# Performance work log

Measured on AMD Instinct MI355X. Metric: run time of the kernel, lower is better.

## Reference

```python
import jax, jax.numpy as jnp
import numpy as np
import math

NUM_HEADS = 16
HEAD_DIM = 64
D_MODEL = NUM_HEADS * HEAD_DIM  # 1024
B, S = 4, 2048

def setup_inputs() -> dict:
    key = jax.random.key(0)
    ks = jax.random.split(key, 8)
    sd = 1.0 / math.sqrt(D_MODEL)
    return {
        "hidden_states": jax.random.normal(ks[0], (B, S, D_MODEL), jnp.float32),
        "attention_mask": jnp.zeros((B, 1, 1, S), jnp.float32),
        "Wq": jax.random.normal(ks[1], (D_MODEL, D_MODEL), jnp.float32) * sd,
        "bq": jnp.zeros((D_MODEL,), jnp.float32),
        "Wk": jax.random.normal(ks[2], (D_MODEL, D_MODEL), jnp.float32) * sd,
        "bk": jnp.zeros((D_MODEL,), jnp.float32),
        "Wv": jax.random.normal(ks[3], (D_MODEL, D_MODEL), jnp.float32) * sd,
        "bv": jnp.zeros((D_MODEL,), jnp.float32),
    }

def _split_heads(x):
    # [B, S, D] -> [B, H, S, hd]
    b, s, _ = x.shape
    return x.reshape(b, s, NUM_HEADS, HEAD_DIM).transpose(0, 2, 1, 3)

def reference(hidden_states, attention_mask, Wq, bq, Wk, bk, Wv, bv):
    # Linear projections (torch nn.Linear: x @ W.T + b)
    q = _split_heads(hidden_states @ Wq.T + bq)
    k = _split_heads(hidden_states @ Wk.T + bk)
    v = _split_heads(hidden_states @ Wv.T + bv)
    scale = 1.0 / math.sqrt(HEAD_DIM)
    # [B, H, Sq, Sk] attention scores, fully materialized as in the original
    scores = jnp.einsum("bhqd,bhkd->bhqk", q, k) * scale + attention_mask
    # relusq replacement for softmax
    probs = jnp.square(jax.nn.relu(scores))
    ctx = jnp.einsum("bhqk,bhkd->bhqd", probs, v)  # [B, H, S, hd]
    b = ctx.shape[0]
    return ctx.transpose(0, 2, 1, 3).reshape(b, -1, D_MODEL)
```

## Files before the change

### kernel.cpp

```cpp
#include <hip/hip_runtime.h>


typedef __bf16 bf16x8 __attribute__((ext_vector_type(8)));
typedef __bf16 bf16x4 __attribute__((ext_vector_type(4)));
typedef short  s16x4  __attribute__((ext_vector_type(4)));
typedef float  f32x4  __attribute__((ext_vector_type(4)));
typedef float  floatx4 __attribute__((ext_vector_type(4)));

#define MFMA16(a, b, c) __builtin_amdgcn_mfma_f32_16x16x32_bf16(a, b, c, 0, 0, 0)
#define MFMA16K16(a, b, c) \
    __builtin_amdgcn_mfma_f32_16x16x16bf16_1k(a, b, c, 0, 0, 0)

#define WAITCNT_VM0() __builtin_amdgcn_s_waitcnt(0x0F70)
#define WAITCNT_VM2() __builtin_amdgcn_s_waitcnt(0x0F72)
#define BARRIER() __builtin_amdgcn_s_barrier()
#define SETPRIO(p) __builtin_amdgcn_s_setprio(p)

__device__ __forceinline__ void glds16(const __bf16* g, __bf16* l) {
    __builtin_amdgcn_global_load_lds(
        (const __attribute__((address_space(1))) void*)g,
        (__attribute__((address_space(3))) void*)l, 16, 0, 0);
}

__global__ __launch_bounds__(256) void convert_kernel(
    const float* __restrict__ X, const float* __restrict__ Wq,
    const float* __restrict__ Wk, const float* __restrict__ Wv,
    __bf16* __restrict__ Xb, __bf16* __restrict__ Wqb,
    __bf16* __restrict__ Wkb, __bf16* __restrict__ Wvb)
{
    int blk = blockIdx.x;
    const float* src; __bf16* dst; size_t base;
    if (blk < 4096)      { src = X;  dst = Xb;  base = (size_t)blk * 2048; }
    else if (blk < 4608) { src = Wq; dst = Wqb; base = (size_t)(blk - 4096) * 2048; }
    else if (blk < 5120) { src = Wk; dst = Wkb; base = (size_t)(blk - 4608) * 2048; }
    else                 { src = Wv; dst = Wvb; base = (size_t)(blk - 5120) * 2048; }
    size_t off = base + (size_t)threadIdx.x * 8;
    floatx4 a = *(const floatx4*)(src + off);
    floatx4 c = *(const floatx4*)(src + off + 4);
    bf16x8 o;
    o[0] = (__bf16)a[0]; o[1] = (__bf16)a[1]; o[2] = (__bf16)a[2]; o[3] = (__bf16)a[3];
    o[4] = (__bf16)c[0]; o[5] = (__bf16)c[1]; o[6] = (__bf16)c[2]; o[7] = (__bf16)c[3];
    *(bf16x8*)(dst + off) = o;
}

__global__ __launch_bounds__(256) void qkv_gemm_kernel(
    const __bf16* __restrict__ Xb,
    const __bf16* __restrict__ Wqb, const __bf16* __restrict__ Wkb,
    const __bf16* __restrict__ Wvb,
    const float* __restrict__ bq, const float* __restrict__ bk,
    const float* __restrict__ bv,
    __bf16* __restrict__ qws, __bf16* __restrict__ kws, __bf16* __restrict__ vws)
{
    __shared__ __bf16 As[2][128 * 64];
    __shared__ __bf16 Bs[2][128 * 64];

    const int tid  = threadIdx.x;
    const int lane = tid & 63;
    const int wave = tid >> 6;
    const int wm   = (wave >> 1) * 64;
    const int wn   = (wave & 1) * 64;
    const int quad = lane >> 4;
    const int l16  = lane & 15;
    const int m0   = blockIdx.y * 128;

    const int sel = blockIdx.x >> 3;
    const bool vmode = (sel == 2);
    const __bf16* Wb = (sel == 0) ? Wqb : (sel == 1) ? Wkb : Wvb;
    const float* bias = (sel == 0) ? bq : (sel == 1) ? bk : bv;
    __bf16* outp = (sel == 0) ? qws : (sel == 1) ? kws : vws;
    const int n0 = (blockIdx.x & 7) * 128;

    const int woffA = vmode ? wm : wn;
    const int woffB = vmode ? wn : wm;

    const int srow = lane >> 3;
    const int schk = lane & 7;

    f32x4 acc[4][4] = {};

    #pragma unroll
    for (int i = 0; i < 4; ++i) {
        int rb = wave * 32 + i * 8;
        int r  = rb + srow;
        int c  = schk ^ (r & 7);
        glds16(Xb + (size_t)(m0 + r) * 1024 + c * 8, &As[0][rb * 64]);
        glds16(Wb + (size_t)(n0 + r) * 1024 + c * 8, &Bs[0][rb * 64]);
    }
    WAITCNT_VM0();
    BARRIER();

    for (int s = 0; s < 16; ++s) {
        const int kn = ((s + 1) & 15) * 64;
        const int nb = (s + 1) & 1;
        const int bc = s & 1;
        #pragma unroll
        for (int i = 0; i < 4; ++i) {
            int rb = wave * 32 + i * 8;
            int r  = rb + srow;
            int c  = schk ^ (r & 7);
            glds16(Xb + (size_t)(m0 + r) * 1024 + kn + c * 8, &As[nb][rb * 64]);
            glds16(Wb + (size_t)(n0 + r) * 1024 + kn + c * 8, &Bs[nb][rb * 64]);
        }

        const __bf16* Pa_ = vmode ? &As[bc][0] : &Bs[bc][0];
        const __bf16* Pb_ = vmode ? &Bs[bc][0] : &As[bc][0];

        SETPRIO(1);
        #pragma unroll
        for (int kk8 = 0; kk8 < 8; kk8 += 4) {
            bf16x8 af[4], bfr[4];
            #pragma unroll
            for (int a = 0; a < 4; ++a)
                af[a] = *(const bf16x8*)&Pa_[(woffA + a * 16 + l16) * 64 +
                                             (((kk8 + quad) ^ (l16 & 7)) * 8)];
            #pragma unroll
            for (int bb = 0; bb < 4; ++bb)
                bfr[bb] = *(const bf16x8*)&Pb_[(woffB + bb * 16 + l16) * 64 +
                                               (((kk8 + quad) ^ (l16 & 7)) * 8)];
            #pragma unroll
            for (int a = 0; a < 4; ++a)
                #pragma unroll
                for (int bb = 0; bb < 4; ++bb)
                    acc[a][bb] = MFMA16(af[a], bfr[bb], acc[a][bb]);
        }
        SETPRIO(0);

        WAITCNT_VM0();
        BARRIER();
    }

    if (!vmode) {
        #pragma unroll
        for (int a = 0; a < 4; ++a) {
            int n = n0 + woffA + a * 16 + quad * 4;
            floatx4 bv4 = *(const floatx4*)&bias[n];
            int h = n >> 6, d0 = n & 63;
            #pragma unroll
            for (int bb = 0; bb < 4; ++bb) {
                int m = m0 + woffB + bb * 16 + l16;
                int bt = m >> 11, ss = m & 2047;
                bf16x4 o;
                #pragma unroll
                for (int r = 0; r < 4; ++r)
                    o[r] = (__bf16)(acc[a][bb][r] + bv4[r]);
                *(bf16x4*)&outp[((size_t)(bt * 16 + h) * 2048 + ss) * 64 + d0] = o;
            }
        }
    } else {
        #pragma unroll
        for (int a = 0; a < 4; ++a) {
            int m = m0 + woffA + a * 16 + quad * 4;
            int bt = m >> 11, s0 = m & 2047;
            #pragma unroll
            for (int bb = 0; bb < 4; ++bb) {
                int n = n0 + woffB + bb * 16 + l16;
                float bvv = bias[n];
                int h = n >> 6, d = n & 63;
                bf16x4 o;
                #pragma unroll
                for (int r = 0; r < 4; ++r)
                    o[r] = (__bf16)(acc[a][bb][r] + bvv);
                *(bf16x4*)&outp[((size_t)(bt * 16 + h) * 64 + d) * 2048 + s0] = o;
            }
        }
    }
}

__global__ __launch_bounds__(512, 4) void attn_kernel(
    const __bf16* __restrict__ Q, const __bf16* __restrict__ K,
    const __bf16* __restrict__ Vt, const float* __restrict__ mask,
    float* __restrict__ out)
{
    __shared__ __bf16 Ks[2][64 * 64];
    __shared__ __bf16 Vs[2][64 * 64];
    __shared__ float  Ms[2048];

    const int tid  = threadIdx.x;
    const int lane = tid & 63;
    const int wave = tid >> 6;
    const int quad = lane >> 4;
    const int l16  = lane & 15;
    const int bh   = blockIdx.x;
    const int b    = bh >> 4;
    const int h    = bh & 15;
    const int q0   = blockIdx.y * 256 + wave * 32;

    const __bf16* Qb = Q  + (size_t)bh * 2048 * 64;
    const __bf16* Kb = K  + (size_t)bh * 2048 * 64;
    const __bf16* Vb = Vt + (size_t)bh * 64 * 2048;
    const float*  mb = mask + b * 2048;

    const int rb = wave * 8;
    const int sr = rb + (lane >> 3);
    const int sc = ((lane & 7) ^ (sr & 7)) * 8;

    bf16x8 aq[2][2];
    #pragma unroll
    for (int qi = 0; qi < 2; ++qi)
        #pragma unroll
        for (int kcd = 0; kcd < 2; ++kcd)
            aq[qi][kcd] = *(const bf16x8*)(Qb +
                (size_t)(q0 + qi * 16 + l16) * 64 + kcd * 32 + quad * 8);

    f32x4 co[2][4] = {};

    glds16(Kb + (size_t)sr * 64 + sc, &Ks[0][rb * 64]);
    glds16(Vb + (size_t)sr * 2048 + sc, &Vs[0][rb * 64]);
    glds16((const __bf16*)mb + (size_t)wave * 512 + lane * 8,
           (__bf16*)Ms + wave * 512);

    for (int t = 0; t < 32; ++t) {
        const int k0 = t * 64;
        const int kn = ((t + 1) & 31) * 64;
        const int nb = (t + 1) & 1;
        glds16(Kb + (size_t)(kn + sr) * 64 + sc, &Ks[nb][rb * 64]);
        glds16(Vb + (size_t)sr * 2048 + kn + sc, &Vs[nb][rb * 64]);
        WAITCNT_VM2();
        BARRIER();

        const __bf16* Kt = &Ks[t & 1][0];
        const __bf16* Vtile = &Vs[t & 1][0];

        f32x4 st[4][2] = {};
        SETPRIO(1);
        #pragma unroll
        for (int ki = 0; ki < 4; ++ki) {
            #pragma unroll
            for (int kcd = 0; kcd < 2; ++kcd) {
                int key = ki * 16 + l16;
                bf16x8 ak = *(const bf16x8*)&Kt[key * 64 +
                    (((kcd * 4 + quad) ^ (key & 7)) * 8)];
                #pragma unroll
                for (int qi = 0; qi < 2; ++qi)
                    st[ki][qi] = MFMA16(ak, aq[qi][kcd], st[ki][qi]);
            }
        }
        SETPRIO(0);

        bf16x4 pf[4][2];
        const f32x4 zero4 = {};
        #pragma unroll
        for (int ki = 0; ki < 4; ++ki) {
            f32x4 mk = *(const f32x4*)&Ms[k0 + ki * 16 + quad * 4];
            #pragma unroll
            for (int qi = 0; qi < 2; ++qi) {
                f32x4 x = st[ki][qi] * 0.125f + mk;
                x = __builtin_elementwise_max(x, zero4);
                x = x * x;
                bf16x4 pv;
                pv[0] = (__bf16)x[0]; pv[1] = (__bf16)x[1];
                pv[2] = (__bf16)x[2]; pv[3] = (__bf16)x[3];
                pf[ki][qi] = pv;
            }
        }

        SETPRIO(1);
        #pragma unroll
        for (int ki = 0; ki < 4; ++ki) {
            bf16x4 vb4[4];
            #pragma unroll
            for (int dt = 0; dt < 4; ++dt) {
                int d = dt * 16 + l16;
                int g = ki * 2 + (quad >> 1);
                vb4[dt] = *(const bf16x4*)&Vtile[d * 64 +
                    ((g ^ (d & 7)) * 8) + (quad & 1) * 4];
            }
            #pragma unroll
            for (int qi = 0; qi < 2; ++qi) {
                s16x4 pa = __builtin_bit_cast(s16x4, pf[ki][qi]);
                #pragma unroll
                for (int dt = 0; dt < 4; ++dt)
                    co[qi][dt] = MFMA16K16(pa,
                        __builtin_bit_cast(s16x4, vb4[dt]), co[qi][dt]);
            }
        }
        SETPRIO(0);
        BARRIER();
    }

    #pragma unroll
    for (int qi = 0; qi < 2; ++qi)
        #pragma unroll
        for (int r = 0; r < 4; ++r) {
            int q = q0 + qi * 16 + quad * 4 + r;
            float* orow = &out[(((size_t)b * 2048 + q) * 16 + h) * 64];
            #pragma unroll
            for (int dt = 0; dt < 4; ++dt)
                orow[dt * 16 + l16] = co[qi][dt][r];
        }
}

extern "C" void kernel_launch(void* const* d_in, const int* in_sizes, int n_in,
                              void* d_out, int out_size, void* d_ws, size_t ws_size,
                              hipStream_t stream) {
    const float* hidden = (const float*)d_in[0];
    const float* mask   = (const float*)d_in[1];
    const float* Wq     = (const float*)d_in[2];
    const float* bq     = (const float*)d_in[3];
    const float* Wk     = (const float*)d_in[4];
    const float* bk     = (const float*)d_in[5];
    const float* Wv     = (const float*)d_in[6];
    const float* bv     = (const float*)d_in[7];
    float* out = (float*)d_out;

    __bf16* qws = (__bf16*)d_ws;
    __bf16* kws = qws + (size_t)64 * 2048 * 64;
    __bf16* vws = kws + (size_t)64 * 2048 * 64;
    __bf16* Xb  = vws + (size_t)64 * 2048 * 64;
    __bf16* Wqb = Xb  + (size_t)8192 * 1024;
    __bf16* Wkb = Wqb + (size_t)1024 * 1024;
    __bf16* Wvb = Wkb + (size_t)1024 * 1024;

    convert_kernel<<<dim3(5632), dim3(256), 0, stream>>>(hidden, Wq, Wk, Wv,
                                                         Xb, Wqb, Wkb, Wvb);
    qkv_gemm_kernel<<<dim3(24, 64), dim3(256), 0, stream>>>(Xb, Wqb, Wkb, Wvb,
                                                            bq, bk, bv,
                                                            qws, kws, vws);
    attn_kernel<<<dim3(64, 8), dim3(512), 0, stream>>>(qws, kws, vws, mask, out);
}
```

Before: 250.2 us.

## Double-buffer 128-key K/V tiles with one barrier per iteration in attention

The attention loop now stages two 64-key K and V sub-tiles per iteration, so it runs 16 iterations instead of 32. Prefetch for the next 128 keys is issued at the top of the loop and waited on at the bottom, with one barrier per iteration, so the global loads can overlap a full iteration of MFMA work instead of being waited on right away. This halves the barrier and waitcnt count. In exchange LDS use doubles to 64KB for K/V plus 8KB for the mask, which may cut the number of resident blocks per CU below the launch-bounds target of 4.

```diff
diff --git a/kernel.cpp b/kernel.cpp
--- a/kernel.cpp
+++ b/kernel.cpp
@@ -12,7 +12,6 @@
     __builtin_amdgcn_mfma_f32_16x16x16bf16_1k(a, b, c, 0, 0, 0)
 
 #define WAITCNT_VM0() __builtin_amdgcn_s_waitcnt(0x0F70)
-#define WAITCNT_VM2() __builtin_amdgcn_s_waitcnt(0x0F72)
 #define BARRIER() __builtin_amdgcn_s_barrier()
 #define SETPRIO(p) __builtin_amdgcn_s_setprio(p)
 
@@ -171,8 +170,8 @@
     const __bf16* __restrict__ Vt, const float* __restrict__ mask,
     float* __restrict__ out)
 {
-    __shared__ __bf16 Ks[2][64 * 64];
-    __shared__ __bf16 Vs[2][64 * 64];
+    __shared__ __bf16 Ks[2][2][64 * 64];
+    __shared__ __bf16 Vs[2][2][64 * 64];
     __shared__ float  Ms[2048];
 
     const int tid  = threadIdx.x;
@@ -204,77 +203,87 @@
 
     f32x4 co[2][4] = {};
 
-    glds16(Kb + (size_t)sr * 64 + sc, &Ks[0][rb * 64]);
-    glds16(Vb + (size_t)sr * 2048 + sc, &Vs[0][rb * 64]);
+    glds16(Kb + (size_t)sr * 64 + sc,        &Ks[0][0][rb * 64]);
+    glds16(Kb + (size_t)(64 + sr) * 64 + sc, &Ks[0][1][rb * 64]);
+    glds16(Vb + (size_t)sr * 2048 + sc,      &Vs[0][0][rb * 64]);
+    glds16(Vb + (size_t)sr * 2048 + 64 + sc, &Vs[0][1][rb * 64]);
     glds16((const __bf16*)mb + (size_t)wave * 512 + lane * 8,
            (__bf16*)Ms + wave * 512);
-
-    for (int t = 0; t < 32; ++t) {
-        const int k0 = t * 64;
-        const int kn = ((t + 1) & 31) * 64;
+    WAITCNT_VM0();
+    BARRIER();
+
+    for (int t = 0; t < 16; ++t) {
+        const int kn = ((t + 1) & 15) * 128;
         const int nb = (t + 1) & 1;
-        glds16(Kb + (size_t)(kn + sr) * 64 + sc, &Ks[nb][rb * 64]);
-        glds16(Vb + (size_t)sr * 2048 + kn + sc, &Vs[nb][rb * 64]);
-        WAITCNT_VM2();
-        BARRIER();
-
-        const __bf16* Kt = &Ks[t & 1][0];
-        const __bf16* Vtile = &Vs[t & 1][0];
-
-        f32x4 st[4][2] = {};
-        SETPRIO(1);
-        #pragma unroll
-        for (int ki = 0; ki < 4; ++ki) {
-            #pragma unroll
-            for (int kcd = 0; kcd < 2; ++kcd) {
-                int key = ki * 16 + l16;
-                bf16x8 ak = *(const bf16x8*)&Kt[key * 64 +
-                    (((kcd * 4 + quad) ^ (key & 7)) * 8)];
-                #pragma unroll
-                for (int qi = 0; qi < 2; ++qi)
-                    st[ki][qi] = MFMA16(ak, aq[qi][kcd], st[ki][qi]);
-            }
-        }
-        SETPRIO(0);
-
-        bf16x4 pf[4][2];
-        const f32x4 zero4 = {};
-        #pragma unroll
-        for (int ki = 0; ki < 4; ++ki) {
-            f32x4 mk = *(const f32x4*)&Ms[k0 + ki * 16 + quad * 4];
-            #pragma unroll
-            for (int qi = 0; qi < 2; ++qi) {
-                f32x4 x = st[ki][qi] * 0.125f + mk;
-                x = __builtin_elementwise_max(x, zero4);
-                x = x * x;
-                bf16x4 pv;
-                pv[0] = (__bf16)x[0]; pv[1] = (__bf16)x[1];
-                pv[2] = (__bf16)x[2]; pv[3] = (__bf16)x[3];
-                pf[ki][qi] = pv;
-            }
-        }
-
-        SETPRIO(1);
-        #pragma unroll
-        for (int ki = 0; ki < 4; ++ki) {
-            bf16x4 vb4[4];
-            #pragma unroll
-            for (int dt = 0; dt < 4; ++dt) {
-                int d = dt * 16 + l16;
-                int g = ki * 2 + (quad >> 1);
-                vb4[dt] = *(const bf16x4*)&Vtile[d * 64 +
-                    ((g ^ (d & 7)) * 8) + (quad & 1) * 4];
-            }
-            #pragma unroll
-            for (int qi = 0; qi < 2; ++qi) {
-                s16x4 pa = __builtin_bit_cast(s16x4, pf[ki][qi]);
-                #pragma unroll
-                for (int dt = 0; dt < 4; ++dt)
-                    co[qi][dt] = MFMA16K16(pa,
-                        __builtin_bit_cast(s16x4, vb4[dt]), co[qi][dt]);
-            }
-        }
-        SETPRIO(0);
+        const int cb = t & 1;
+        glds16(Kb + (size_t)(kn + sr) * 64 + sc,       &Ks[nb][0][rb * 64]);
+        glds16(Kb + (size_t)(kn + 64 + sr) * 64 + sc,  &Ks[nb][1][rb * 64]);
+        glds16(Vb + (size_t)sr * 2048 + kn + sc,       &Vs[nb][0][rb * 64]);
+        glds16(Vb + (size_t)sr * 2048 + kn + 64 + sc,  &Vs[nb][1][rb * 64]);
+
+        #pragma unroll
+        for (int hf = 0; hf < 2; ++hf) {
+            const __bf16* Kt = &Ks[cb][hf][0];
+            const __bf16* Vtile = &Vs[cb][hf][0];
+            const int k0 = t * 128 + hf * 64;
+
+            f32x4 st[4][2] = {};
+            SETPRIO(1);
+            #pragma unroll
+            for (int ki = 0; ki < 4; ++ki) {
+                #pragma unroll
+                for (int kcd = 0; kcd < 2; ++kcd) {
+                    int key = ki * 16 + l16;
+                    bf16x8 ak = *(const bf16x8*)&Kt[key * 64 +
+                        (((kcd * 4 + quad) ^ (key & 7)) * 8)];
+                    #pragma unroll
+                    for (int qi = 0; qi < 2; ++qi)
+                        st[ki][qi] = MFMA16(ak, aq[qi][kcd], st[ki][qi]);
+                }
+            }
+            SETPRIO(0);
+
+            bf16x4 pf[4][2];
+            const f32x4 zero4 = {};
+            #pragma unroll
+            for (int ki = 0; ki < 4; ++ki) {
+                f32x4 mk = *(const f32x4*)&Ms[k0 + ki * 16 + quad * 4];
+                #pragma unroll
+                for (int qi = 0; qi < 2; ++qi) {
+                    f32x4 x = st[ki][qi] * 0.125f + mk;
+                    x = __builtin_elementwise_max(x, zero4);
+                    x = x * x;
+                    bf16x4 pv;
+                    pv[0] = (__bf16)x[0]; pv[1] = (__bf16)x[1];
+                    pv[2] = (__bf16)x[2]; pv[3] = (__bf16)x[3];
+                    pf[ki][qi] = pv;
+                }
+            }
+
+            SETPRIO(1);
+            #pragma unroll
+            for (int ki = 0; ki < 4; ++ki) {
+                bf16x4 vb4[4];
+                #pragma unroll
+                for (int dt = 0; dt < 4; ++dt) {
+                    int d = dt * 16 + l16;
+                    int g = ki * 2 + (quad >> 1);
+                    vb4[dt] = *(const bf16x4*)&Vtile[d * 64 +
+                        ((g ^ (d & 7)) * 8) + (quad & 1) * 4];
+                }
+                #pragma unroll
+                for (int qi = 0; qi < 2; ++qi) {
+                    s16x4 pa = __builtin_bit_cast(s16x4, pf[ki][qi]);
+                    #pragma unroll
+                    for (int dt = 0; dt < 4; ++dt)
+                        co[qi][dt] = MFMA16K16(pa,
+                            __builtin_bit_cast(s16x4, vb4[dt]), co[qi][dt]);
+                }
+            }
+            SETPRIO(0);
+        }
+
+        WAITCNT_VM0();
         BARRIER();
     }
 
```

After: 250.4 us. Within noise of the previous version (+0.1%).
